# Performance work log

Measured on AMD Instinct MI355X. Metric: run time of the kernel, lower is better.

Reference implementation:

```python
import jax, jax.numpy as jnp
import numpy as np

EPS = 1e-10


def _log_scaling(feats):
    """Raw feats (..., 15): xmin,ymin,xmax,ymax,area,angle,pca_big,pca_small,hu1..hu7
    -> (..., 17): xmin..area, log|pca_big..hu7|, lshape, cosangle, sinangle."""
    lshape = jnp.sqrt(feats[..., 7:8]) / (jnp.sqrt(feats[..., 6:7]) + EPS)
    cosangle = jnp.cos(feats[..., 5:6])
    sinangle = jnp.sin(feats[..., 5:6])
    logged = jnp.log(jnp.abs(feats[..., 5:]) + EPS)  # cols 5..14 logged
    # original drops the (logged) angle column 5 and keeps logged cols 6..14
    return jnp.concatenate([feats[..., :5], logged[..., 1:], lshape, cosangle, sinangle], axis=-1)


def _make_parents(n_trees, P, seed=0):
    """Valid topologically-ordered tree: parent[p] < p, parent[0] = 0 (root)."""
    rng = np.random.default_rng(seed)
    idx = np.arange(P)
    high = np.maximum(idx, 1)
    par = rng.integers(0, 2**31 - 1, size=(n_trees, P)) % high[None, :]
    par[:, 0] = 0
    return par.astype(np.int32)


def setup_inputs() -> dict:
    key = jax.random.key(0)
    k1, k2, k3, k4 = jax.random.split(key, 4)
    B, N, H, W = 2, 2, 1024, 1024
    P = H * W
    x = jax.random.normal(k1, (B, N, H, W), dtype=jnp.float32) * 10.0
    weight = jax.random.uniform(k2, (N, 17, 1), dtype=jnp.float32, minval=-0.01, maxval=0.01)
    bias = jnp.zeros((N, 1), dtype=jnp.float32)
    attrs = jax.random.uniform(k3, (B, N, P, 15), dtype=jnp.float32) * 4.0
    parents = jnp.asarray(_make_parents(B * N, P).reshape(B, N, P))
    return {"x": x, "weight": weight, "bias": bias, "attrs": attrs, "parents": parents}


def _path_sum(contrib_pad, par_pad, P):
    """Pointer-doubling root-to-node path sums over a tree with sentinel at index P."""
    iters = max(int(np.ceil(np.log2(max(P, 2)))), 1)

    def body(i, carry):
        v, p = carry
        return v + v[p], p[p]

    v, _ = jax.lax.fori_loop(0, iters, body, (contrib_pad, par_pad))
    return v[:P]


def reference(x, weight, bias, attrs, parents):
    B, N, H, W = x.shape
    P = H * W
    xf = x.reshape(B, N, P)
    idx = jnp.arange(P, dtype=parents.dtype)
    is_root = parents == idx  # (B,N,P)
    parent_vals = jnp.take_along_axis(xf, parents, axis=-1)
    diff = jnp.where(is_root, xf, xf - parent_vals)  # per-node gray-level increment
    feats = _log_scaling(attrs)  # (B,N,P,17)
    lin = jnp.einsum('bnpf,nfo->bnpo', feats, weight) + bias[None, :, None, :]
    scores = jax.nn.sigmoid(lin[..., 0])  # (B,N,P)
    contrib = diff * scores
    # sentinel node P with contribution 0; roots point at the sentinel
    sent = jnp.full((B, N, 1), P, dtype=parents.dtype)
    par_pad = jnp.concatenate([jnp.where(is_root, P, parents), sent], axis=-1)
    contrib_pad = jnp.concatenate([contrib, jnp.zeros((B, N, 1), x.dtype)], axis=-1)
    out = jax.vmap(jax.vmap(lambda c, p: _path_sum(c, p, P)))(contrib_pad, par_pad)
    return out.reshape(B, N, H, W)
```

## Files before the change

### kernel.cpp

```cpp
#include <hip/hip_runtime.h>
#include <math.h>

#define EPSF 1e-10f
#define P_NODES (1 << 20)

struct __align__(8) NodePair {
    float v;
    int   par;
};

__global__ __launch_bounds__(256) void score_kernel(
    const float* __restrict__ x,
    const float* __restrict__ weight,
    const float* __restrict__ bias,
    const float* __restrict__ attrs,
    const int*   __restrict__ parents,
    NodePair*    __restrict__ dst,
    int N)
{
    __shared__ float sA[256 * 15];

    const int t = threadIdx.x;
    const int blockBase = blockIdx.x * 256;
    const int idx = blockBase + t;

    const float* ab = attrs + (size_t)blockBase * 15;
#pragma unroll
    for (int j = 0; j < 15; ++j)
        sA[j * 256 + t] = ab[j * 256 + t];

    const int tree = blockBase >> 20;
    const int n    = tree % N;
    const float* w = weight + n * 17;
    const float  b = bias[n];

    __syncthreads();

    const float* a = &sA[t * 15];

    float acc = b;
    acc += a[0] * w[0];
    acc += a[1] * w[1];
    acc += a[2] * w[2];
    acc += a[3] * w[3];
    acc += a[4] * w[4];

    const float a5 = a[5];
    const float a6 = a[6];
    const float a7 = a[7];

    acc += __logf(fabsf(a6)    + EPSF) * w[5];
    acc += __logf(fabsf(a7)    + EPSF) * w[6];
    acc += __logf(fabsf(a[8])  + EPSF) * w[7];
    acc += __logf(fabsf(a[9])  + EPSF) * w[8];
    acc += __logf(fabsf(a[10]) + EPSF) * w[9];
    acc += __logf(fabsf(a[11]) + EPSF) * w[10];
    acc += __logf(fabsf(a[12]) + EPSF) * w[11];
    acc += __logf(fabsf(a[13]) + EPSF) * w[12];
    acc += __logf(fabsf(a[14]) + EPSF) * w[13];

    const float lshape = __fsqrt_rn(a7) / (__fsqrt_rn(a6) + EPSF);
    acc += lshape * w[14];
    acc += __cosf(a5) * w[15];
    acc += __sinf(a5) * w[16];

    const float score = 1.0f / (1.0f + __expf(-acc));

    const int   p   = idx & (P_NODES - 1);
    const int   par = parents[idx];
    const float xv  = x[idx];

    NodePair r;
    if (par == p) {
        r.v   = xv * score;
        r.par = -1;
    } else {
        r.v   = (xv - x[(idx - p) + par]) * score;
        r.par = par;
    }
    dst[idx] = r;
}

__global__ __launch_bounds__(256) void jump_kernel(
    const NodePair* __restrict__ src,
    NodePair*       __restrict__ dst,
    int nHalf)
{
    const int i = blockIdx.x * blockDim.x + threadIdx.x;
    if (i >= nHalf) return;

    const int idx0 = i * 2;
    const int base = idx0 & ~(P_NODES - 1);

    float4 r = ((const float4*)src)[i];
    float v0 = r.x;  int p0 = __float_as_int(r.y);
    float v1 = r.z;  int p1 = __float_as_int(r.w);

    if (p0 >= 0) {
        NodePair q = src[base + p0];
        v0 += q.v;  p0 = q.par;
    }
    if (p1 >= 0) {
        NodePair q = src[base + p1];
        v1 += q.v;  p1 = q.par;
    }

    float4 o;
    o.x = v0; o.y = __int_as_float(p0);
    o.z = v1; o.w = __int_as_float(p1);
    ((float4*)dst)[i] = o;
}

__global__ __launch_bounds__(256) void final_kernel(
    const NodePair* __restrict__ src,
    float*          __restrict__ out,
    int nHalf)
{
    const int i = blockIdx.x * blockDim.x + threadIdx.x;
    if (i >= nHalf) return;

    const int idx0 = i * 2;
    const int base = idx0 & ~(P_NODES - 1);

    float4 r = ((const float4*)src)[i];

    float s0 = r.x;  int c0 = __float_as_int(r.y);
    while (c0 >= 0) {
        NodePair q = src[base + c0];
        s0 += q.v;  c0 = q.par;
    }
    float s1 = r.z;  int c1 = __float_as_int(r.w);
    while (c1 >= 0) {
        NodePair q = src[base + c1];
        s1 += q.v;  c1 = q.par;
    }

    float2 o; o.x = s0; o.y = s1;
    ((float2*)out)[i] = o;
}

extern "C" void kernel_launch(void* const* d_in, const int* in_sizes, int n_in,
                              void* d_out, int out_size, void* d_ws, size_t ws_size,
                              hipStream_t stream)
{
    const float* x       = (const float*)d_in[0];
    const float* weight  = (const float*)d_in[1];
    const float* bias    = (const float*)d_in[2];
    const float* attrs   = (const float*)d_in[3];
    const int*   parents = (const int*)d_in[4];
    float*       out     = (float*)d_out;

    const int total = in_sizes[0];
    const int N     = in_sizes[1] / 17;

    NodePair* bufA = (NodePair*)d_ws;
    NodePair* bufB = (NodePair*)((char*)d_ws + (size_t)total * sizeof(NodePair));

    const int block = 256;
    const int grid  = (total + block - 1) / block;
    const int nHalf = total / 2;
    const int gridH = (nHalf + block - 1) / block;

    score_kernel<<<grid, block, 0, stream>>>(x, weight, bias, attrs, parents,
                                             bufA, N);
    jump_kernel<<<gridH, block, 0, stream>>>(bufA, bufB, nHalf);
    jump_kernel<<<gridH, block, 0, stream>>>(bufB, bufA, nHalf);
    jump_kernel<<<gridH, block, 0, stream>>>(bufA, bufB, nHalf);
    jump_kernel<<<gridH, block, 0, stream>>>(bufB, bufA, nHalf);
    final_kernel<<<gridH, block, 0, stream>>>(bufA, out, nHalf);
}
```

Measured before the change: 486.4 us.

## Replace pointer-jumping passes with frontier prefix sums plus short chain resolve

```diff
diff --git a/kernel.cpp b/kernel.cpp
--- a/kernel.cpp
+++ b/kernel.cpp
@@ -3,6 +3,7 @@
 
 #define EPSF 1e-10f
 #define P_NODES (1 << 20)
+#define T_FRONT 65536
 
 struct __align__(8) NodePair {
     float v;
@@ -81,38 +82,32 @@
     dst[idx] = r;
 }
 
-__global__ __launch_bounds__(256) void jump_kernel(
-    const NodePair* __restrict__ src,
-    NodePair*       __restrict__ dst,
-    int nHalf)
+__global__ __launch_bounds__(256) void frontier_kernel(
+    const NodePair* __restrict__ pairs,
+    float*          __restrict__ S,
+    int nTrees)
 {
     const int i = blockIdx.x * blockDim.x + threadIdx.x;
-    if (i >= nHalf) return;
+    if (i >= nTrees * T_FRONT) return;
 
-    const int idx0 = i * 2;
-    const int base = idx0 & ~(P_NODES - 1);
+    const int tree = i / T_FRONT;
+    const int p    = i - tree * T_FRONT;
+    const int base = tree << 20;
 
-    float4 r = ((const float4*)src)[i];
-    float v0 = r.x;  int p0 = __float_as_int(r.y);
-    float v1 = r.z;  int p1 = __float_as_int(r.w);
-
-    if (p0 >= 0) {
-        NodePair q = src[base + p0];
-        v0 += q.v;  p0 = q.par;
+    NodePair r = pairs[base + p];
+    float s = r.v;
+    int   c = r.par;
+    while (c >= 0) {
+        NodePair q = pairs[base + c];
+        s += q.v;
+        c  = q.par;
     }
-    if (p1 >= 0) {
-        NodePair q = src[base + p1];
-        v1 += q.v;  p1 = q.par;
-    }
-
-    float4 o;
-    o.x = v0; o.y = __int_as_float(p0);
-    o.z = v1; o.w = __int_as_float(p1);
-    ((float4*)dst)[i] = o;
+    S[i] = s;
 }
 
-__global__ __launch_bounds__(256) void final_kernel(
-    const NodePair* __restrict__ src,
+__global__ __launch_bounds__(256) void resolve_kernel(
+    const NodePair* __restrict__ pairs,
+    const float*    __restrict__ S,
     float*          __restrict__ out,
     int nHalf)
 {
@@ -121,19 +116,24 @@
 
     const int idx0 = i * 2;
     const int base = idx0 & ~(P_NODES - 1);
+    const int tree = idx0 >> 20;
+    const float* St = S + (size_t)tree * T_FRONT;
 
-    float4 r = ((const float4*)src)[i];
+    float4 r = ((const float4*)pairs)[i];
+    float s0 = r.x;  int c0 = __float_as_int(r.y);
+    float s1 = r.z;  int c1 = __float_as_int(r.w);
 
-    float s0 = r.x;  int c0 = __float_as_int(r.y);
-    while (c0 >= 0) {
-        NodePair q = src[base + c0];
-        s0 += q.v;  c0 = q.par;
+    bool a0 = (c0 >= T_FRONT);
+    bool a1 = (c1 >= T_FRONT);
+    while (a0 || a1) {
+        NodePair q0, q1;
+        if (a0) q0 = pairs[base + c0];
+        if (a1) q1 = pairs[base + c1];
+        if (a0) { s0 += q0.v; c0 = q0.par; a0 = (c0 >= T_FRONT); }
+        if (a1) { s1 += q1.v; c1 = q1.par; a1 = (c1 >= T_FRONT); }
     }
-    float s1 = r.z;  int c1 = __float_as_int(r.w);
-    while (c1 >= 0) {
-        NodePair q = src[base + c1];
-        s1 += q.v;  c1 = q.par;
-    }
+    if (c0 >= 0) s0 += St[c0];
+    if (c1 >= 0) s1 += St[c1];
 
     float2 o; o.x = s0; o.y = s1;
     ((float2*)out)[i] = o;
@@ -150,22 +150,22 @@
     const int*   parents = (const int*)d_in[4];
     float*       out     = (float*)d_out;
 
-    const int total = in_sizes[0];
-    const int N     = in_sizes[1] / 17;
+    const int total  = in_sizes[0];
+    const int N      = in_sizes[1] / 17;
+    const int nTrees = total >> 20;
 
-    NodePair* bufA = (NodePair*)d_ws;
-    NodePair* bufB = (NodePair*)((char*)d_ws + (size_t)total * sizeof(NodePair));
+    NodePair* pairs = (NodePair*)d_ws;
+    float*    S     = (float*)((char*)d_ws + (size_t)total * sizeof(NodePair));
 
     const int block = 256;
     const int grid  = (total + block - 1) / block;
     const int nHalf = total / 2;
     const int gridH = (nHalf + block - 1) / block;
+    const int nF    = nTrees * T_FRONT;
+    const int gridF = (nF + block - 1) / block;
 
     score_kernel<<<grid, block, 0, stream>>>(x, weight, bias, attrs, parents,
-                                             bufA, N);
-    jump_kernel<<<gridH, block, 0, stream>>>(bufA, bufB, nHalf);
-    jump_kernel<<<gridH, block, 0, stream>>>(bufB, bufA, nHalf);
-    jump_kernel<<<gridH, block, 0, stream>>>(bufA, bufB, nHalf);
-    jump_kernel<<<gridH, block, 0, stream>>>(bufB, bufA, nHalf);
-    final_kernel<<<gridH, block, 0, stream>>>(bufA, out, nHalf);
+                                             pairs, N);
+    frontier_kernel<<<gridF, block, 0, stream>>>(pairs, S, nTrees);
+    resolve_kernel<<<gridH, block, 0, stream>>>(pairs, S, out, nHalf);
 }
```

Result: faster. 440.6 us (-9.4%).
